# Kernel tuning notes

Measured on AMD Instinct MI355X. Metric: run time of the kernel, lower is better.

Reference implementation:

```python
import jax, jax.numpy as jnp
import numpy as np

TEMPERATURE = 0.07
EPS = 1e-8          # torch cosine_similarity norm clamp
DIAG_FILL = 9e-15   # value masked_fill'ed onto the diagonal BEFORE temperature scaling


def setup_inputs() -> dict:
    key = jax.random.key(0)
    N, D = 16384, 128
    feats = jax.random.normal(key, (N, D), dtype=jnp.float32)
    # unique labels: required for the original torch code's broadcast
    # (-cos_sim[pos_mask] must have exactly N elements)
    labels = jnp.arange(N, dtype=jnp.int32).reshape(N, 1)
    return {"feats": feats, "labels": labels}


def reference(feats, labels):
    # cosine similarity matrix: normalize rows once, then a single GEMM
    norm = jnp.maximum(jnp.linalg.norm(feats, axis=-1, keepdims=True), EPS)
    f = feats / norm
    cos_sim = f @ f.T                                   # [N, N]

    N = cos_sim.shape[0]
    eye = jnp.eye(N, dtype=bool)
    cos_sim = jnp.where(eye, DIAG_FILL, cos_sim)        # masked_fill_(self_mask, 9e-15)
    cos_sim = cos_sim / TEMPERATURE

    pos_mask = labels == labels.T                       # [N, N] bool, one True per row
    # cos_sim[pos_mask] with exactly one positive per row == masked row-sum
    pos = jnp.sum(jnp.where(pos_mask, cos_sim, 0.0), axis=-1)  # [N]

    nll = -pos + jax.nn.logsumexp(cos_sim, axis=-1)     # [N]
    return jnp.mean(nll)
```

## Files before the change

kernel.cpp:

```cpp
#include <hip/hip_runtime.h>
#include <hip/hip_bf16.h>
#include <stdint.h>

typedef __attribute__((ext_vector_type(8))) short short8;
typedef __attribute__((ext_vector_type(4))) float f32x4;

#define N_ROWS 16384
#define DIM 128

constexpr float ALPHA = 4.5398160f;
constexpr float POSC = 1.2857143e-13f;

__device__ __forceinline__ void gload_lds16(const void* g, void* lds) {
  __builtin_amdgcn_global_load_lds(
      (const __attribute__((address_space(1))) void*)(uintptr_t)g,
      (__attribute__((address_space(3))) void*)(uintptr_t)lds,
      16, 0, 0);
}

__global__ void normalize_kernel(const float* __restrict__ feats,
                                 unsigned short* __restrict__ G,
                                 float* __restrict__ rowsum) {
  const int tid  = threadIdx.x;
  const int lane = tid & 63;
  const int row  = blockIdx.x * 4 + (tid >> 6);

  const float2 v = *(const float2*)(feats + (size_t)row * DIM + lane * 2);
  float ss = v.x * v.x + v.y * v.y;
#pragma unroll
  for (int m = 1; m < 64; m <<= 1) ss += __shfl_xor(ss, m);
  const float sc = ALPHA / fmaxf(sqrtf(ss), 1e-8f);

  __hip_bfloat16 h0 = __float2bfloat16(v.x * sc);
  __hip_bfloat16 h1 = __float2bfloat16(v.y * sc);
  unsigned int packed = (unsigned int)(*(unsigned short*)&h0) |
                        ((unsigned int)(*(unsigned short*)&h1) << 16);
  *(unsigned int*)(G + (size_t)row * DIM + lane * 2) = packed;

  if (blockIdx.x < 64) rowsum[blockIdx.x * 256 + tid] = 0.f;
}

__global__ __launch_bounds__(256, 2) void simclr_lse_kernel(
    const unsigned short* __restrict__ G, float* __restrict__ rowsum) {
  const int tid  = threadIdx.x;
  const int lane = tid & 63;
  const int w    = tid >> 6;
  const int wr   = w >> 1;
  const int wc   = w & 1;
  const int c    = lane & 15;
  const int q    = lane >> 4;

  const int rt      = blockIdx.x & 127;
  const int seg     = blockIdx.x >> 7;
  const int rowBase = rt * 128;

  __shared__ __align__(16) unsigned short Bbuf[128 * 128];
  __shared__ float ldsRow[128];

  if (tid < 128) ldsRow[tid] = 0.f;

  short8 afrag[4][4];
  {
    const short* Gs = (const short*)G;
    const int rbw = rowBase + wr * 64;
#pragma unroll
    for (int tr = 0; tr < 4; ++tr)
#pragma unroll
      for (int ks = 0; ks < 4; ++ks) {
        const int row = rbw + tr * 16 + c;
        afrag[tr][ks] = *(const short8*)(Gs + (size_t)row * DIM + ks * 32 + q * 8);
      }
  }

  unsigned boff[4][4];
#pragma unroll
  for (int tc = 0; tc < 4; ++tc)
#pragma unroll
    for (int ks = 0; ks < 4; ++ks) {
      const int col = wc * 64 + tc * 16 + c;
      const int kc  = ks * 4 + q;
      boff[tc][ks] = (unsigned)((col * 16 + (kc ^ c)) * 16);
    }

  unsigned goff[8];
#pragma unroll
  for (int t = 0; t < 8; ++t) {
    const int cidx = t * 256 + tid;
    const int col  = cidx >> 4;
    const int kc   = (cidx & 15) ^ (col & 15);
    goff[t] = (unsigned)(col * DIM + kc * 8);
  }

  float rs[4][4];
#pragma unroll
  for (int tr = 0; tr < 4; ++tr)
#pragma unroll
    for (int r = 0; r < 4; ++r) rs[tr][r] = 0.f;

  const f32x4 zero4 = {0.f, 0.f, 0.f, 0.f};
  const char* bbase = (const char*)Bbuf;

  for (int ch = 0; ch < 32; ++ch) {
    const int cb = seg * 4096 + ch * 128;
    __syncthreads();
    {
      const unsigned short* gsrc = G + (size_t)cb * DIM;
#pragma unroll
      for (int t = 0; t < 8; ++t)
        gload_lds16(gsrc + goff[t], (void*)(Bbuf + (size_t)(t * 256 + w * 64) * 8));
    }
    __syncthreads();

    f32x4 acc[4][4];
#pragma unroll
    for (int ks = 0; ks < 4; ++ks) {
      short8 bfr[4];
#pragma unroll
      for (int tc = 0; tc < 4; ++tc)
        bfr[tc] = *(const short8*)(bbase + boff[tc][ks]);
#pragma unroll
      for (int tr = 0; tr < 4; ++tr)
#pragma unroll
        for (int tc = 0; tc < 4; ++tc) {
          if (ks == 0)
            acc[tr][tc] = __builtin_amdgcn_mfma_f32_16x16x32_bf16(
                afrag[tr][0], bfr[tc], zero4, 0, 0, 0);
          else
            acc[tr][tc] = __builtin_amdgcn_mfma_f32_16x16x32_bf16(
                afrag[tr][ks], bfr[tc], acc[tr][tc], 0, 0, 0);
        }
    }

    if (cb == rowBase && wr == wc) {
#pragma unroll
      for (int tr = 0; tr < 4; ++tr)
#pragma unroll
        for (int r = 0; r < 4; ++r)
          if (c == q * 4 + r) acc[tr][tr][r] = 0.f;
    }

#pragma unroll
    for (int tr = 0; tr < 4; ++tr)
#pragma unroll
      for (int r = 0; r < 4; ++r) {
        float s = rs[tr][r];
#pragma unroll
        for (int tc = 0; tc < 4; ++tc)
          s += __builtin_amdgcn_exp2f(acc[tr][tc][r]);
        rs[tr][r] = s;
      }
  }

#pragma unroll
  for (int tr = 0; tr < 4; ++tr)
#pragma unroll
    for (int r = 0; r < 4; ++r) {
      float v = rs[tr][r];
      v += __shfl_xor(v, 1);
      v += __shfl_xor(v, 2);
      v += __shfl_xor(v, 4);
      v += __shfl_xor(v, 8);
      rs[tr][r] = v;
    }
  if (c == 0) {
#pragma unroll
    for (int tr = 0; tr < 4; ++tr)
#pragma unroll
      for (int r = 0; r < 4; ++r)
        atomicAdd(&ldsRow[wr * 64 + tr * 16 + q * 4 + r], rs[tr][r]);
  }
  __syncthreads();
  if (tid < 128) atomicAdd(&rowsum[rowBase + tid], ldsRow[tid]);
}

__global__ void finalize_kernel(const float* __restrict__ rowsum,
                                float* __restrict__ out) {
  const int tid = threadIdx.x;
  float local = 0.f;
  for (int i = tid; i < N_ROWS; i += 1024) local += logf(rowsum[i]);
#pragma unroll
  for (int m = 1; m < 64; m <<= 1) local += __shfl_xor(local, m);
  __shared__ float part[16];
  if ((tid & 63) == 0) part[tid >> 6] = local;
  __syncthreads();
  if (tid == 0) {
    float s = 0.f;
#pragma unroll
    for (int i = 0; i < 16; ++i) s += part[i];
    out[0] = s / (float)N_ROWS - POSC;
  }
}

extern "C" void kernel_launch(void* const* d_in, const int* in_sizes, int n_in,
                              void* d_out, int out_size, void* d_ws, size_t ws_size,
                              hipStream_t stream) {
  (void)in_sizes; (void)n_in; (void)out_size; (void)ws_size;
  const float* feats = (const float*)d_in[0];
  unsigned short* G = (unsigned short*)d_ws;
  float* rowsum = (float*)((char*)d_ws + (size_t)N_ROWS * DIM * 2);

  normalize_kernel<<<dim3(N_ROWS / 4), dim3(256), 0, stream>>>(feats, G, rowsum);
  simclr_lse_kernel<<<dim3(512), dim3(256), 0, stream>>>(G, rowsum);
  finalize_kernel<<<dim3(1), dim3(1024), 0, stream>>>(rowsum, d_out ? (float*)d_out : nullptr);
}
```

Measured before the change: 131.4 us.

## Exploit Gram matrix symmetry with triangular tile schedule and LDS double buffering

Computes only the upper-triangular 128x128 tiles of the symmetric similarity matrix. Each tile's exponentials feed both row sums and column sums, with the column sums pushed to global memory by atomics. Blocks pair row tile p with row tile 127-p so every block gets an equal share of tiles. The B tile load is double-buffered so the next tile's global-to-LDS copy overlaps the current MFMA work. This roughly halves the MFMA and exp work, in exchange for many more global atomics and twice the LDS per block, which may reduce occupancy.

```diff
diff --git a/kernel.cpp b/kernel.cpp
--- a/kernel.cpp
+++ b/kernel.cpp
@@ -50,37 +50,14 @@
   const int c    = lane & 15;
   const int q    = lane >> 4;
 
-  const int rt      = blockIdx.x & 127;
-  const int seg     = blockIdx.x >> 7;
-  const int rowBase = rt * 128;
-
-  __shared__ __align__(16) unsigned short Bbuf[128 * 128];
-  __shared__ float ldsRow[128];
-
-  if (tid < 128) ldsRow[tid] = 0.f;
-
-  short8 afrag[4][4];
-  {
-    const short* Gs = (const short*)G;
-    const int rbw = rowBase + wr * 64;
-#pragma unroll
-    for (int tr = 0; tr < 4; ++tr)
-#pragma unroll
-      for (int ks = 0; ks < 4; ++ks) {
-        const int row = rbw + tr * 16 + c;
-        afrag[tr][ks] = *(const short8*)(Gs + (size_t)row * DIM + ks * 32 + q * 8);
-      }
-  }
-
-  unsigned boff[4][4];
-#pragma unroll
-  for (int tc = 0; tc < 4; ++tc)
-#pragma unroll
-    for (int ks = 0; ks < 4; ++ks) {
-      const int col = wc * 64 + tc * 16 + c;
-      const int kc  = ks * 4 + q;
-      boff[tc][ks] = (unsigned)((col * 16 + (kc ^ c)) * 16);
-    }
+  const int p  = blockIdx.x >> 3;
+  const int s  = blockIdx.x & 7;
+  const int r8 = p & 7;
+  const int jb = (s * 129 + r8) >> 3;
+  const int je = ((s + 1) * 129 + r8) >> 3;
+  const int split = 128 - p;
+
+  __shared__ __align__(16) unsigned short Bbuf[2][128 * 128];
 
   unsigned goff[8];
 #pragma unroll
@@ -91,86 +68,141 @@
     goff[t] = (unsigned)(col * DIM + kc * 8);
   }
 
-  float rs[4][4];
-#pragma unroll
-  for (int tr = 0; tr < 4; ++tr)
-#pragma unroll
-    for (int r = 0; r < 4; ++r) rs[tr][r] = 0.f;
+  unsigned boff[4][4];
+#pragma unroll
+  for (int tc = 0; tc < 4; ++tc)
+#pragma unroll
+    for (int ks = 0; ks < 4; ++ks) {
+      const int col = wc * 64 + tc * 16 + c;
+      const int kc  = ks * 4 + q;
+      boff[tc][ks] = (unsigned)((col * 16 + (kc ^ c)) * 16);
+    }
 
   const f32x4 zero4 = {0.f, 0.f, 0.f, 0.f};
-  const char* bbase = (const char*)Bbuf;
-
-  for (int ch = 0; ch < 32; ++ch) {
-    const int cb = seg * 4096 + ch * 128;
+  const short* Gs = (const short*)G;
+
+  for (int sg = 0; sg < 2; ++sg) {
+    int rt, cbeg, nct;
+    if (sg == 0) {
+      rt   = p;
+      cbeg = p + jb;
+      nct  = min(je, split) - jb;
+    } else {
+      rt   = 127 - p;
+      const int t0 = max(jb, split);
+      cbeg = t0 - 1;
+      nct  = je - t0;
+    }
+    if (nct <= 0) continue;
+
+    const int rbw = rt * 128 + wr * 64;
+
+    short8 afrag[4][4];
+#pragma unroll
+    for (int tr = 0; tr < 4; ++tr)
+#pragma unroll
+      for (int ks = 0; ks < 4; ++ks) {
+        const int row = rbw + tr * 16 + c;
+        afrag[tr][ks] = *(const short8*)(Gs + (size_t)row * DIM + ks * 32 + q * 8);
+      }
+
+    float rs[4][4];
+#pragma unroll
+    for (int tr = 0; tr < 4; ++tr)
+#pragma unroll
+      for (int r = 0; r < 4; ++r) rs[tr][r] = 0.f;
+
+    {
+      const unsigned short* gsrc = G + (size_t)cbeg * 128 * DIM;
+#pragma unroll
+      for (int t = 0; t < 8; ++t)
+        gload_lds16(gsrc + goff[t],
+                    (void*)(&Bbuf[0][0] + (size_t)(t * 256 + w * 64) * 8));
+    }
+
+    for (int jj = 0; jj < nct; ++jj) {
+      const int cur = jj & 1;
+      const int ct  = cbeg + jj;
+      __syncthreads();
+
+      if (jj + 1 < nct) {
+        const unsigned short* gsrc = G + (size_t)(ct + 1) * 128 * DIM;
+#pragma unroll
+        for (int t = 0; t < 8; ++t)
+          gload_lds16(gsrc + goff[t],
+                      (void*)(&Bbuf[cur ^ 1][0] + (size_t)(t * 256 + w * 64) * 8));
+      }
+
+      const char* bbase = (const char*)&Bbuf[cur][0];
+      f32x4 acc[4][4];
+#pragma unroll
+      for (int ks = 0; ks < 4; ++ks) {
+        short8 bfr[4];
+#pragma unroll
+        for (int tc = 0; tc < 4; ++tc)
+          bfr[tc] = *(const short8*)(bbase + boff[tc][ks]);
+#pragma unroll
+        for (int tr = 0; tr < 4; ++tr)
+#pragma unroll
+          for (int tc = 0; tc < 4; ++tc) {
+            if (ks == 0)
+              acc[tr][tc] = __builtin_amdgcn_mfma_f32_16x16x32_bf16(
+                  afrag[tr][0], bfr[tc], zero4, 0, 0, 0);
+            else
+              acc[tr][tc] = __builtin_amdgcn_mfma_f32_16x16x32_bf16(
+                  afrag[tr][ks], bfr[tc], acc[tr][tc], 0, 0, 0);
+          }
+      }
+
+      if (ct == rt && wr == wc) {
+#pragma unroll
+        for (int tr = 0; tr < 4; ++tr)
+#pragma unroll
+          for (int r = 0; r < 4; ++r)
+            if (c == q * 4 + r) acc[tr][tr][r] = 0.f;
+      }
+
+      float cs[4] = {0.f, 0.f, 0.f, 0.f};
+#pragma unroll
+      for (int tr = 0; tr < 4; ++tr)
+#pragma unroll
+        for (int tc = 0; tc < 4; ++tc) {
+          const float e0 = __builtin_amdgcn_exp2f(acc[tr][tc][0]);
+          const float e1 = __builtin_amdgcn_exp2f(acc[tr][tc][1]);
+          const float e2 = __builtin_amdgcn_exp2f(acc[tr][tc][2]);
+          const float e3 = __builtin_amdgcn_exp2f(acc[tr][tc][3]);
+          rs[tr][0] += e0;
+          rs[tr][1] += e1;
+          rs[tr][2] += e2;
+          rs[tr][3] += e3;
+          cs[tc] += (e0 + e1) + (e2 + e3);
+        }
+
+      if (ct != rt) {
+#pragma unroll
+        for (int tc = 0; tc < 4; ++tc) {
+          float v = cs[tc];
+          v += __shfl_xor(v, 16);
+          v += __shfl_xor(v, 32);
+          if (q == 0)
+            atomicAdd(&rowsum[ct * 128 + wc * 64 + tc * 16 + c], v);
+        }
+      }
+    }
+
+#pragma unroll
+    for (int tr = 0; tr < 4; ++tr)
+#pragma unroll
+      for (int r = 0; r < 4; ++r) {
+        float v = rs[tr][r];
+        v += __shfl_xor(v, 1);
+        v += __shfl_xor(v, 2);
+        v += __shfl_xor(v, 4);
+        v += __shfl_xor(v, 8);
+        if (c == 0) atomicAdd(&rowsum[rbw + tr * 16 + q * 4 + r], v);
+      }
     __syncthreads();
-    {
-      const unsigned short* gsrc = G + (size_t)cb * DIM;
-#pragma unroll
-      for (int t = 0; t < 8; ++t)
-        gload_lds16(gsrc + goff[t], (void*)(Bbuf + (size_t)(t * 256 + w * 64) * 8));
-    }
-    __syncthreads();
-
-    f32x4 acc[4][4];
-#pragma unroll
-    for (int ks = 0; ks < 4; ++ks) {
-      short8 bfr[4];
-#pragma unroll
-      for (int tc = 0; tc < 4; ++tc)
-        bfr[tc] = *(const short8*)(bbase + boff[tc][ks]);
-#pragma unroll
-      for (int tr = 0; tr < 4; ++tr)
-#pragma unroll
-        for (int tc = 0; tc < 4; ++tc) {
-          if (ks == 0)
-            acc[tr][tc] = __builtin_amdgcn_mfma_f32_16x16x32_bf16(
-                afrag[tr][0], bfr[tc], zero4, 0, 0, 0);
-          else
-            acc[tr][tc] = __builtin_amdgcn_mfma_f32_16x16x32_bf16(
-                afrag[tr][ks], bfr[tc], acc[tr][tc], 0, 0, 0);
-        }
-    }
-
-    if (cb == rowBase && wr == wc) {
-#pragma unroll
-      for (int tr = 0; tr < 4; ++tr)
-#pragma unroll
-        for (int r = 0; r < 4; ++r)
-          if (c == q * 4 + r) acc[tr][tr][r] = 0.f;
-    }
-
-#pragma unroll
-    for (int tr = 0; tr < 4; ++tr)
-#pragma unroll
-      for (int r = 0; r < 4; ++r) {
-        float s = rs[tr][r];
-#pragma unroll
-        for (int tc = 0; tc < 4; ++tc)
-          s += __builtin_amdgcn_exp2f(acc[tr][tc][r]);
-        rs[tr][r] = s;
-      }
   }
-
-#pragma unroll
-  for (int tr = 0; tr < 4; ++tr)
-#pragma unroll
-    for (int r = 0; r < 4; ++r) {
-      float v = rs[tr][r];
-      v += __shfl_xor(v, 1);
-      v += __shfl_xor(v, 2);
-      v += __shfl_xor(v, 4);
-      v += __shfl_xor(v, 8);
-      rs[tr][r] = v;
-    }
-  if (c == 0) {
-#pragma unroll
-    for (int tr = 0; tr < 4; ++tr)
-#pragma unroll
-      for (int r = 0; r < 4; ++r)
-        atomicAdd(&ldsRow[wr * 64 + tr * 16 + q * 4 + r], rs[tr][r]);
-  }
-  __syncthreads();
-  if (tid < 128) atomicAdd(&rowsum[rowBase + tid], ldsRow[tid]);
 }
 
 __global__ void finalize_kernel(const float* __restrict__ rowsum,
```

Result: faster. 116.6 us (-11.3%).

## Exploit Gram matrix symmetry to compute only lower-triangular tiles

Applied to the files above, without the earlier changes.

The similarity matrix is symmetric, so only the lower-triangular 128x128 tile pairs are computed. Each tile's exponentials feed the row sums of the row tile and, through column reductions, the row sums of the column tile. This roughly halves MFMA and exp work. In exchange it adds per-tile global atomics, an irregular triangular work split across 884 blocks, and a launch bound raised to 4 blocks per CU.

```diff
diff --git a/kernel.cpp b/kernel.cpp
--- a/kernel.cpp
+++ b/kernel.cpp
@@ -40,7 +40,7 @@
   if (blockIdx.x < 64) rowsum[blockIdx.x * 256 + tid] = 0.f;
 }
 
-__global__ __launch_bounds__(256, 2) void simclr_lse_kernel(
+__global__ __launch_bounds__(256, 4) void simclr_lse_kernel(
     const unsigned short* __restrict__ G, float* __restrict__ rowsum) {
   const int tid  = threadIdx.x;
   const int lane = tid & 63;
@@ -50,37 +50,23 @@
   const int c    = lane & 15;
   const int q    = lane >> 4;
 
-  const int rt      = blockIdx.x & 127;
-  const int seg     = blockIdx.x >> 7;
-  const int rowBase = rt * 128;
-
-  __shared__ __align__(16) unsigned short Bbuf[128 * 128];
-  __shared__ float ldsRow[128];
-
-  if (tid < 128) ldsRow[tid] = 0.f;
-
-  short8 afrag[4][4];
+  int ct, k;
   {
-    const short* Gs = (const short*)G;
-    const int rbw = rowBase + wr * 64;
-#pragma unroll
-    for (int tr = 0; tr < 4; ++tr)
-#pragma unroll
-      for (int ks = 0; ks < 4; ++ks) {
-        const int row = rbw + tr * 16 + c;
-        afrag[tr][ks] = *(const short8*)(Gs + (size_t)row * DIM + ks * 32 + q * 8);
-      }
-  }
-
-  unsigned boff[4][4];
-#pragma unroll
-  for (int tc = 0; tc < 4; ++tc)
-#pragma unroll
-    for (int ks = 0; ks < 4; ++ks) {
-      const int col = wc * 64 + tc * 16 + c;
-      const int kc  = ks * 4 + q;
-      boff[tc][ks] = (unsigned)((col * 16 + (kc ^ c)) * 16);
-    }
+    int bid = blockIdx.x, a = 0;
+    for (;;) {
+      const int cols = (a < 12) ? 10 : 8;
+      const int span = cols * (a + 1);
+      if (bid < span) { ct = a * 10 + bid / (a + 1); k = bid % (a + 1); break; }
+      bid -= span; ++a;
+    }
+  }
+  const int n   = ct + 1;
+  const int m   = ct / 10 + 1;
+  const int sz  = n / m, rem = n % m;
+  const int lo  = k * sz + min(k, rem);
+  const int len = sz + (k < rem ? 1 : 0);
+
+  __shared__ __align__(16) unsigned short Tbuf[128 * 128];
 
   unsigned goff[8];
 #pragma unroll
@@ -91,47 +77,68 @@
     goff[t] = (unsigned)(col * DIM + kc * 8);
   }
 
-  float rs[4][4];
+  unsigned aoff[4][4];
 #pragma unroll
   for (int tr = 0; tr < 4; ++tr)
 #pragma unroll
-    for (int r = 0; r < 4; ++r) rs[tr][r] = 0.f;
+    for (int ks = 0; ks < 4; ++ks) {
+      const int line = wr * 64 + tr * 16 + c;
+      const int kc   = ks * 4 + q;
+      aoff[tr][ks] = (unsigned)((line * 16 + (kc ^ c)) * 16);
+    }
+
+  {
+    const unsigned short* gsrc = G + (size_t)ct * 128 * DIM;
+#pragma unroll
+    for (int t = 0; t < 8; ++t)
+      gload_lds16(gsrc + goff[t], (void*)(Tbuf + (size_t)(t * 256 + w * 64) * 8));
+  }
+  __syncthreads();
+  short8 bfr[4][4];
+#pragma unroll
+  for (int tc = 0; tc < 4; ++tc)
+#pragma unroll
+    for (int ks = 0; ks < 4; ++ks) {
+      const int line = wc * 64 + tc * 16 + c;
+      const int kc   = ks * 4 + q;
+      bfr[tc][ks] = *(const short8*)((const char*)Tbuf + (line * 16 + (kc ^ c)) * 16);
+    }
 
   const f32x4 zero4 = {0.f, 0.f, 0.f, 0.f};
-  const char* bbase = (const char*)Bbuf;
-
-  for (int ch = 0; ch < 32; ++ch) {
-    const int cb = seg * 4096 + ch * 128;
+  float csAcc[4] = {0.f, 0.f, 0.f, 0.f};
+
+  for (int j = 0; j < len; ++j) {
+    const int rt = lo + j;
     __syncthreads();
     {
-      const unsigned short* gsrc = G + (size_t)cb * DIM;
+      const unsigned short* gsrc = G + (size_t)rt * 128 * DIM;
 #pragma unroll
       for (int t = 0; t < 8; ++t)
-        gload_lds16(gsrc + goff[t], (void*)(Bbuf + (size_t)(t * 256 + w * 64) * 8));
+        gload_lds16(gsrc + goff[t], (void*)(Tbuf + (size_t)(t * 256 + w * 64) * 8));
     }
     __syncthreads();
 
     f32x4 acc[4][4];
 #pragma unroll
     for (int ks = 0; ks < 4; ++ks) {
-      short8 bfr[4];
-#pragma unroll
-      for (int tc = 0; tc < 4; ++tc)
-        bfr[tc] = *(const short8*)(bbase + boff[tc][ks]);
+      short8 afr[4];
+#pragma unroll
+      for (int tr = 0; tr < 4; ++tr)
+        afr[tr] = *(const short8*)((const char*)Tbuf + aoff[tr][ks]);
 #pragma unroll
       for (int tr = 0; tr < 4; ++tr)
 #pragma unroll
         for (int tc = 0; tc < 4; ++tc) {
           if (ks == 0)
             acc[tr][tc] = __builtin_amdgcn_mfma_f32_16x16x32_bf16(
-                afrag[tr][0], bfr[tc], zero4, 0, 0, 0);
+                afr[tr], bfr[tc][0], zero4, 0, 0, 0);
           else
             acc[tr][tc] = __builtin_amdgcn_mfma_f32_16x16x32_bf16(
-                afrag[tr][ks], bfr[tc], acc[tr][tc], 0, 0, 0);
+                afr[tr], bfr[tc][ks], acc[tr][tc], 0, 0, 0);
         }
     }
 
-    if (cb == rowBase && wr == wc) {
+    if (rt == ct && wr == wc) {
 #pragma unroll
       for (int tr = 0; tr < 4; ++tr)
 #pragma unroll
@@ -139,38 +146,46 @@
           if (c == q * 4 + r) acc[tr][tr][r] = 0.f;
     }
 
+    float rs[4][4];
+    const bool mirror = (rt != ct);
 #pragma unroll
     for (int tr = 0; tr < 4; ++tr)
 #pragma unroll
+      for (int tc = 0; tc < 4; ++tc) {
+        const float e0 = __builtin_amdgcn_exp2f(acc[tr][tc][0]);
+        const float e1 = __builtin_amdgcn_exp2f(acc[tr][tc][1]);
+        const float e2 = __builtin_amdgcn_exp2f(acc[tr][tc][2]);
+        const float e3 = __builtin_amdgcn_exp2f(acc[tr][tc][3]);
+        if (tc == 0) {
+          rs[tr][0] = e0; rs[tr][1] = e1; rs[tr][2] = e2; rs[tr][3] = e3;
+        } else {
+          rs[tr][0] += e0; rs[tr][1] += e1; rs[tr][2] += e2; rs[tr][3] += e3;
+        }
+        if (mirror) csAcc[tc] += (e0 + e1) + (e2 + e3);
+      }
+
+#pragma unroll
+    for (int tr = 0; tr < 4; ++tr)
+#pragma unroll
       for (int r = 0; r < 4; ++r) {
-        float s = rs[tr][r];
-#pragma unroll
-        for (int tc = 0; tc < 4; ++tc)
-          s += __builtin_amdgcn_exp2f(acc[tr][tc][r]);
-        rs[tr][r] = s;
+        float v = rs[tr][r];
+        v += __shfl_xor(v, 1);
+        v += __shfl_xor(v, 2);
+        v += __shfl_xor(v, 4);
+        v += __shfl_xor(v, 8);
+        if (c == 0)
+          atomicAdd(&rowsum[rt * 128 + wr * 64 + tr * 16 + q * 4 + r], v);
       }
   }
 
 #pragma unroll
-  for (int tr = 0; tr < 4; ++tr)
-#pragma unroll
-    for (int r = 0; r < 4; ++r) {
-      float v = rs[tr][r];
-      v += __shfl_xor(v, 1);
-      v += __shfl_xor(v, 2);
-      v += __shfl_xor(v, 4);
-      v += __shfl_xor(v, 8);
-      rs[tr][r] = v;
-    }
-  if (c == 0) {
-#pragma unroll
-    for (int tr = 0; tr < 4; ++tr)
-#pragma unroll
-      for (int r = 0; r < 4; ++r)
-        atomicAdd(&ldsRow[wr * 64 + tr * 16 + q * 4 + r], rs[tr][r]);
-  }
-  __syncthreads();
-  if (tid < 128) atomicAdd(&rowsum[rowBase + tid], ldsRow[tid]);
+  for (int tc = 0; tc < 4; ++tc) {
+    float v = csAcc[tc];
+    v += __shfl_xor(v, 16);
+    v += __shfl_xor(v, 32);
+    if (q == 0)
+      atomicAdd(&rowsum[ct * 128 + wc * 64 + tc * 16 + c], v);
+  }
 }
 
 __global__ void finalize_kernel(const float* __restrict__ rowsum,
@@ -200,6 +215,6 @@
   float* rowsum = (float*)((char*)d_ws + (size_t)N_ROWS * DIM * 2);
 
   normalize_kernel<<<dim3(N_ROWS / 4), dim3(256), 0, stream>>>(feats, G, rowsum);
-  simclr_lse_kernel<<<dim3(512), dim3(256), 0, stream>>>(G, rowsum);
+  simclr_lse_kernel<<<dim3(884), dim3(256), 0, stream>>>(G, rowsum);
   finalize_kernel<<<dim3(1), dim3(1024), 0, stream>>>(rowsum, d_out ? (float*)d_out : nullptr);
 }
```

Measured after the change: 263.2 us. +100.3%, slower.
